# Optimization experiments

Hardware: AMD Instinct MI355X
Metric: run time of the kernel (lower is better)

## Reference

```python
import jax, jax.numpy as jnp
import numpy as np

N, E, IN, HID, H, OUT = 50000, 800000, 128, 64, 4, 128
NEG = 0.2   # LeakyReLU slope in GATv2
EPS = 1e-5  # BatchNorm eps


def _seg_softmax(a, seg, n):
    # numerically stable softmax over edges grouped by destination node
    amax = jax.lax.stop_gradient(jax.ops.segment_max(a, seg, num_segments=n))
    amax = jnp.where(jnp.isfinite(amax), amax, 0.0)
    ex = jnp.exp(a - amax[seg])
    den = jax.ops.segment_sum(ex, seg, num_segments=n)
    return ex / (den[seg] + 1e-16)


def _gatv2(x, src, dst, e_attr, Wl, bl, Wr, br, We, att, bias, heads, c, concat):
    n = x.shape[0]
    xl = (x @ Wl + bl).reshape(n, heads, c)   # source transform (x_j)
    xr = (x @ Wr + br).reshape(n, heads, c)   # target transform (x_i)
    ee = (e_attr @ We).reshape(-1, heads, c)  # edge feature transform
    m = xl[src] + xr[dst] + ee                # [E, H, C]
    m = jnp.where(m > 0, m, NEG * m)          # LeakyReLU
    alpha = _seg_softmax(jnp.einsum('ehc,hc->eh', m, att), dst, n)  # [E, H]
    out = jax.ops.segment_sum(alpha[:, :, None] * xl[src], dst, num_segments=n)
    out = out.reshape(n, heads * c) if concat else out.mean(axis=1)
    return out + bias


def _bn(h, g, b):  # BatchNorm1d, training-mode batch stats (biased var)
    mu = jnp.mean(h, axis=0)
    var = jnp.var(h, axis=0)
    return (h - mu) * jax.lax.rsqrt(var + EPS) * g + b


def _prelu(h, a):
    return jnp.where(h > 0, h, a * h)


def setup_inputs() -> dict:
    key = jax.random.key(0)
    ks = jax.random.split(key, 16)
    def nrm(k, shape, fan):
        return jax.random.normal(k, shape, jnp.float32) / np.float32(np.sqrt(fan))
    x = jax.random.normal(ks[0], (N, IN), jnp.float32)
    edge_index = jax.random.randint(ks[1], (2, E), 0, N, jnp.int32)
    edge_attr = jax.random.uniform(ks[2], (E, 1), dtype=jnp.float32)
    return {
        'x': x, 'edge_index': edge_index, 'edge_attr': edge_attr,
        # layer 1: heads=4, concat=True
        'Wl1': nrm(ks[3], (IN, H * HID), IN), 'bl1': jnp.zeros((H * HID,), jnp.float32),
        'Wr1': nrm(ks[4], (IN, H * HID), IN), 'br1': jnp.zeros((H * HID,), jnp.float32),
        'We1': nrm(ks[5], (1, H * HID), 1),
        'att1': nrm(ks[6], (H, HID), HID),
        'cb1': jnp.zeros((H * HID,), jnp.float32),
        'bng1': jnp.ones((H * HID,), jnp.float32), 'bnb1': jnp.zeros((H * HID,), jnp.float32),
        'pa': jnp.float32(0.25),  # PReLU single parameter (shared by both uses)
        # layer 2: heads=1, concat=False
        'Wl2': nrm(ks[7], (H * HID, OUT), H * HID), 'bl2': jnp.zeros((OUT,), jnp.float32),
        'Wr2': nrm(ks[8], (H * HID, OUT), H * HID), 'br2': jnp.zeros((OUT,), jnp.float32),
        'We2': nrm(ks[9], (1, OUT), 1),
        'att2': nrm(ks[10], (1, OUT), OUT),
        'cb2': jnp.zeros((OUT,), jnp.float32),
        'bng2': jnp.ones((OUT,), jnp.float32), 'bnb2': jnp.zeros((OUT,), jnp.float32),
        'skipW': nrm(ks[11], (IN, OUT), IN), 'skipb': jnp.zeros((OUT,), jnp.float32),
    }


def reference(x, edge_index, edge_attr, Wl1, bl1, Wr1, br1, We1, att1, cb1,
              bng1, bnb1, pa, Wl2, bl2, Wr2, br2, We2, att2, cb2, bng2, bnb2,
              skipW, skipb):
    src, dst = edge_index[0], edge_index[1]
    h = _gatv2(x, src, dst, edge_attr, Wl1, bl1, Wr1, br1, We1, att1, cb1, H, HID, True)
    h = _prelu(_bn(h, bng1, bnb1), pa)  # dropout = identity (eval)
    h = _gatv2(h, src, dst, edge_attr, Wl2, bl2, Wr2, br2, We2, att2, cb2, 1, OUT, False)
    h = _prelu(_bn(h, bng2, bnb2), pa)
    return h + (x @ skipW + skipb)
```

## Files before the change

### kernel.cpp

```cpp
#include <hip/hip_runtime.h>
#include <cstdint>
#include <cstddef>

#define NNODES 50000
#define NEDGES 800000
#define DH1    256
#define DOUT   128

typedef unsigned short u16;
typedef __bf16 bf16x8 __attribute__((ext_vector_type(8)));
typedef float  f32x4  __attribute__((ext_vector_type(4)));

__device__ __forceinline__ float bf2f(unsigned int u) {
  union { unsigned int i; float f; } x; x.i = u << 16; return x.f;
}
__device__ __forceinline__ u16 f2bf(float f) {
  union { float f; unsigned int i; } x; x.f = f;
  unsigned int r = x.i + 0x7fffu + ((x.i >> 16) & 1u);
  return (u16)(r >> 16);
}
__device__ __forceinline__ void dec8(uint4 r, float* o) {
  o[0] = bf2f(r.x & 0xffffu); o[1] = bf2f(r.x >> 16);
  o[2] = bf2f(r.y & 0xffffu); o[3] = bf2f(r.y >> 16);
  o[4] = bf2f(r.z & 0xffffu); o[5] = bf2f(r.z >> 16);
  o[6] = bf2f(r.w & 0xffffu); o[7] = bf2f(r.w >> 16);
}
__device__ __forceinline__ uint4 pack8(const float* v) {
  uint4 p;
  p.x = (unsigned)f2bf(v[0]) | ((unsigned)f2bf(v[1]) << 16);
  p.y = (unsigned)f2bf(v[2]) | ((unsigned)f2bf(v[3]) << 16);
  p.z = (unsigned)f2bf(v[4]) | ((unsigned)f2bf(v[5]) << 16);
  p.w = (unsigned)f2bf(v[6]) | ((unsigned)f2bf(v[7]) << 16);
  return p;
}


__global__ __launch_bounds__(256) void count_k(const int* __restrict__ dst, int* __restrict__ cnt) {
  int e = blockIdx.x * 256 + threadIdx.x;
  if (e < NEDGES) atomicAdd(&cnt[dst[e]], 1);
}

__global__ __launch_bounds__(256) void offsets_k(const int* __restrict__ cnt, int* __restrict__ offs,
                                                 int* __restrict__ cursor, int* __restrict__ total) {
  int i = blockIdx.x * 256 + threadIdx.x;
  int lane = threadIdx.x & 63;
  int c = (i < NNODES) ? cnt[i] : 0;
  int incl = c;
  #pragma unroll
  for (int d = 1; d < 64; d <<= 1) {
    int t = __shfl_up(incl, d, 64);
    if (lane >= d) incl += t;
  }
  int wtotal = __shfl(incl, 63, 64);
  int base = 0;
  if (lane == 63) base = atomicAdd(total, wtotal);
  base = __shfl(base, 63, 64);
  int off = base + incl - c;
  if (i < NNODES) { offs[i] = off; cursor[i] = off; }
}

__global__ __launch_bounds__(256) void scatter_k(const int* __restrict__ src, const int* __restrict__ dst,
                                                 const float* __restrict__ ea, int* __restrict__ cursor,
                                                 int2* __restrict__ epair) {
  int e = blockIdx.x * 256 + threadIdx.x;
  if (e >= NEDGES) return;
  int d = dst[e];
  int p = atomicAdd(&cursor[d], 1);
  int2 v; v.x = src[e]; v.y = __float_as_int(ea[e]);
  epair[p] = v;
}


__global__ __launch_bounds__(256) void cvt_bf_k(const float* __restrict__ in, u16* __restrict__ out, int total) {
  int i = (blockIdx.x * 256 + threadIdx.x) * 4;
  if (i >= total) return;
  float4 v = *reinterpret_cast<const float4*>(in + i);
  uint2 pk;
  pk.x = (unsigned)f2bf(v.x) | ((unsigned)f2bf(v.y) << 16);
  pk.y = (unsigned)f2bf(v.z) | ((unsigned)f2bf(v.w) << 16);
  *reinterpret_cast<uint2*>(out + i) = pk;
}

__global__ __launch_bounds__(256) void prep_all_k(
    const float* __restrict__ Wl1, const float* __restrict__ Wr1,
    const float* __restrict__ bl1, const float* __restrict__ br1,
    const float* __restrict__ Wl2, const float* __restrict__ Wr2,
    const float* __restrict__ bl2, const float* __restrict__ br2,
    const float* __restrict__ skW, const float* __restrict__ skb,
    u16* __restrict__ Wt1, float* __restrict__ bias1,
    u16* __restrict__ Wt2, float* __restrict__ bias2,
    u16* __restrict__ Wts, float* __restrict__ biasS) {
  int idx = blockIdx.x * 256 + threadIdx.x;
  int which = blockIdx.y;
  if (which == 0) {
    if (idx < 512) bias1[idx] = (idx < 256) ? bl1[idx] : br1[idx - 256];
    int n = idx >> 7, k = idx & 127;
    float v = (n < 256) ? Wl1[k * 256 + n] : Wr1[k * 256 + (n - 256)];
    Wt1[idx] = f2bf(v);
  } else if (which == 1) {
    if (idx < 256) bias2[idx] = (idx < 128) ? bl2[idx] : br2[idx - 128];
    int n = idx >> 8, k = idx & 255;
    float v = (n < 128) ? Wl2[k * 128 + n] : Wr2[k * 128 + (n - 128)];
    Wt2[idx] = f2bf(v);
  } else {
    if (idx < 128) biasS[idx] = skb[idx];
    if (idx < 128 * 128) {
      int n = idx >> 7, k = idx & 127;
      Wts[idx] = f2bf(skW[k * 128 + n]);
    }
  }
}


template<int K, int NH, int NTOT, bool OUT_BF16>
__global__ __launch_bounds__(512) void gemm_mfma(
    const u16* __restrict__ A, const u16* __restrict__ Wt, const float* __restrict__ bias,
    void* __restrict__ C0v, void* __restrict__ C1v) {
  constexpr int LDA = K + 8;
  constexpr int LD1 = (NTOT - NH) > 0 ? (NTOT - NH) : 1;
  constexpr int CSTR = OUT_BF16 ? 136 : 132;
  constexpr size_t ABYTES = (size_t)64 * LDA * 2;
  constexpr size_t CBYTES = (size_t)64 * CSTR * (OUT_BF16 ? 2 : 4);
  constexpr size_t SBYTES = ABYTES > CBYTES ? ABYTES : CBYTES;
  __shared__ __align__(16) char smem[SBYTES];
  u16* As = (u16*)smem;
  const int row0 = blockIdx.x * 64;
  const int tid = threadIdx.x;
  #pragma unroll
  for (int it = 0; it < K / 32; ++it) {
    int chunk = it * 512 + tid;
    int row = (chunk * 4) / K;
    int col = (chunk * 4) % K;
    uint2 v; v.x = 0u; v.y = 0u;
    int gr = row0 + row;
    if (gr < NNODES) v = *reinterpret_cast<const uint2*>(A + (size_t)gr * K + col);
    *reinterpret_cast<uint2*>(&As[row * LDA + col]) = v;
  }
  __syncthreads();
  const int w = tid >> 6, lane = tid & 63, q = lane >> 4, l16 = lane & 15;
  const int tc = w * 16 + l16;
  const int ncol = blockIdx.y * 128 + tc;
  f32x4 acc[4];
  #pragma unroll
  for (int rt = 0; rt < 4; ++rt) acc[rt] = (f32x4){0.f, 0.f, 0.f, 0.f};
  const u16* wp = Wt + (size_t)ncol * K + q * 8;
  #pragma unroll
  for (int ks = 0; ks < K / 32; ++ks) {
    bf16x8 b = *reinterpret_cast<const bf16x8*>(wp + ks * 32);
    #pragma unroll
    for (int rt = 0; rt < 4; ++rt) {
      bf16x8 a = *reinterpret_cast<const bf16x8*>(&As[(rt * 16 + l16) * LDA + ks * 32 + q * 8]);
      acc[rt] = __builtin_amdgcn_mfma_f32_16x16x32_bf16(a, b, acc[rt], 0, 0, 0);
    }
  }
  const float bval = bias[ncol];
  __syncthreads();
  if constexpr (OUT_BF16) {
    u16* Cs = (u16*)smem;
    #pragma unroll
    for (int rt = 0; rt < 4; ++rt)
      #pragma unroll
      for (int r = 0; r < 4; ++r)
        Cs[(rt * 16 + q * 4 + r) * CSTR + tc] = f2bf(acc[rt][r] + bval);
  } else {
    float* Cs = (float*)smem;
    #pragma unroll
    for (int rt = 0; rt < 4; ++rt)
      #pragma unroll
      for (int r = 0; r < 4; ++r)
        Cs[(rt * 16 + q * 4 + r) * CSTR + tc] = acc[rt][r] + bval;
  }
  __syncthreads();
  const int cb = blockIdx.y * 128;
  const bool first = (cb < NH);
  const int LD = first ? NH : LD1;
  const int cc = first ? cb : (cb - NH);
  if constexpr (OUT_BF16) {
    u16* Cg = (u16*)(first ? C0v : C1v);
    constexpr int CPR = 16;
    #pragma unroll
    for (int it = 0; it < 64 * CPR / 512; ++it) {
      int ch = it * 512 + tid;
      int row = ch / CPR, co = (ch % CPR) * 8;
      int grow = row0 + row;
      if (grow < NNODES) {
        uint4 v = *reinterpret_cast<const uint4*>(&((u16*)smem)[row * CSTR + co]);
        *reinterpret_cast<uint4*>(Cg + (size_t)grow * LD + cc + co) = v;
      }
    }
  } else {
    float* Cg = (float*)(first ? C0v : C1v);
    constexpr int CPR = 32;
    #pragma unroll
    for (int it = 0; it < 64 * CPR / 512; ++it) {
      int ch = it * 512 + tid;
      int row = ch / CPR, co = (ch % CPR) * 4;
      int grow = row0 + row;
      if (grow < NNODES) {
        float4 v = *reinterpret_cast<const float4*>(&((float*)smem)[row * CSTR + co]);
        *reinterpret_cast<float4*>(Cg + (size_t)grow * LD + cc + co) = v;
      }
    }
  }
}


template<int HEADS, int CHAN>
__global__ __launch_bounds__(256) void gat_edge(
    const int* __restrict__ offs, const int* __restrict__ cnt,
    const int2* __restrict__ epair,
    const u16* __restrict__ xl, const u16* __restrict__ xr,
    const float* __restrict__ att, const float* __restrict__ We,
    const float* __restrict__ cb, u16* __restrict__ hout) {
  constexpr int HC  = HEADS * CHAN;
  constexpr int CPL = HC / 16;
  constexpr int NCH = CPL / 8;
  constexpr int LPH = CHAN / CPL;
  static_assert(NCH * 8 == CPL && LPH * CPL == CHAN, "layout");

  int node = __builtin_amdgcn_readfirstlane((int)(blockIdx.x * 4 + (threadIdx.x >> 6)));
  if (node >= NNODES) return;
  const int lane = threadIdx.x & 63;
  const int g    = lane >> 4;
  const int l16  = lane & 15;
  const int cbase = l16 * CPL;

  float xrv[CPL], attv[CPL], wev[CPL];
  {
    const uint4* xrp = reinterpret_cast<const uint4*>(xr + (size_t)node * HC + cbase);
    #pragma unroll
    for (int c = 0; c < NCH; ++c) dec8(xrp[c], &xrv[c * 8]);
    #pragma unroll
    for (int c = 0; c < CPL / 4; ++c) {
      float4 a = *reinterpret_cast<const float4*>(att + cbase + c * 4);
      float4 w = *reinterpret_cast<const float4*>(We  + cbase + c * 4);
      attv[c*4+0] = a.x; attv[c*4+1] = a.y; attv[c*4+2] = a.z; attv[c*4+3] = a.w;
      wev [c*4+0] = w.x; wev [c*4+1] = w.y; wev [c*4+2] = w.z; wev [c*4+3] = w.w;
    }
  }
  const int off = __builtin_amdgcn_readfirstlane(offs[node]);
  const int deg = __builtin_amdgcn_readfirstlane(cnt[node]);

  float den = 0.f;
  float accv[CPL];
  #pragma unroll
  for (int j = 0; j < CPL; ++j) accv[j] = 0.f;

  if (deg > 0) {
    const int last = deg - 1;
    auto midx = [&](int i) { int j = i * 4 + g; return off + (j < last ? j : last); };
    auto rowp = [&](int s) { return reinterpret_cast<const uint4*>(xl + (size_t)s * HC + cbase); };
    const int niter = (deg + 3) >> 2;
    int2 p_cur = epair[midx(0)];
    int2 p_nxt = epair[midx(1)];
    uint4 r_cur[NCH], r_nxt[NCH];
    { const uint4* rp = rowp(p_cur.x);
      #pragma unroll
      for (int c = 0; c < NCH; ++c) r_cur[c] = rp[c]; }
    for (int i = 0; i < niter; ++i) {
      int2 p_n2 = epair[midx(i + 2)];
      { const uint4* rp = rowp(p_nxt.x);
        #pragma unroll
        for (int c = 0; c < NCH; ++c) r_nxt[c] = rp[c]; }
      float ea = __int_as_float(p_cur.y);
      float xlv[CPL];
      #pragma unroll
      for (int c = 0; c < NCH; ++c) dec8(r_cur[c], &xlv[c * 8]);
      float part = 0.f;
      #pragma unroll
      for (int jj = 0; jj < CPL; ++jj) {
        float m = xlv[jj] + xrv[jj] + ea * wev[jj];
        m = m > 0.f ? m : 0.2f * m;
        part += m * attv[jj];
      }
      #pragma unroll
      for (int d = 1; d < LPH; d <<= 1) part += __shfl_xor(part, d, 64);
      float valid = (i * 4 + g <= last) ? 1.f : 0.f;
      float e = __expf(part) * valid;
      den += e;
      #pragma unroll
      for (int jj = 0; jj < CPL; ++jj) accv[jj] += e * xlv[jj];
      p_cur = p_nxt; p_nxt = p_n2;
      #pragma unroll
      for (int c = 0; c < NCH; ++c) r_cur[c] = r_nxt[c];
    }
  }
  den += __shfl_xor(den, 16, 64);
  den += __shfl_xor(den, 32, 64);
  #pragma unroll
  for (int jj = 0; jj < CPL; ++jj) {
    accv[jj] += __shfl_xor(accv[jj], 16, 64);
    accv[jj] += __shfl_xor(accv[jj], 32, 64);
  }
  if (g == 0) {
    float inv = 1.0f / (den + 1e-16f);
    float ov[CPL];
    #pragma unroll
    for (int c = 0; c < CPL / 4; ++c) {
      float4 cv = *reinterpret_cast<const float4*>(cb + cbase + c * 4);
      ov[c*4+0] = accv[c*4+0] * inv + cv.x;
      ov[c*4+1] = accv[c*4+1] * inv + cv.y;
      ov[c*4+2] = accv[c*4+2] * inv + cv.z;
      ov[c*4+3] = accv[c*4+3] * inv + cv.w;
    }
    uint4* op = reinterpret_cast<uint4*>(hout + (size_t)node * HC + cbase);
    #pragma unroll
    for (int c = 0; c < NCH; ++c) op[c] = pack8(&ov[c * 8]);
  }
}


template<int NC>
__global__ void bn_stats_bf(const u16* __restrict__ h, float* __restrict__ sum, float* __restrict__ sq) {
  int c = threadIdx.x;
  float s = 0.f, q = 0.f;
  for (int r = blockIdx.x; r < NNODES; r += gridDim.x) {
    float v = bf2f(h[(size_t)r * NC + c]);
    s += v; q += v * v;
  }
  atomicAdd(&sum[c], s);
  atomicAdd(&sq[c], q);
}

template<int NC>
__global__ __launch_bounds__(256) void bn_prelu_apply(
    const u16* __restrict__ h, const float* __restrict__ sum, const float* __restrict__ sq,
    const float* __restrict__ g, const float* __restrict__ bb_,
    const float* __restrict__ pap, u16* __restrict__ outp, int total) {
  int i = (blockIdx.x * 256 + threadIdx.x) * 4;
  if (i >= total) return;
  const float invN = 1.0f / (float)NNODES;
  float pa = pap[0];
  int c = i & (NC - 1);
  float4 sm = *reinterpret_cast<const float4*>(sum + c);
  float4 qq = *reinterpret_cast<const float4*>(sq + c);
  float4 gg = *reinterpret_cast<const float4*>(g + c);
  float4 bb = *reinterpret_cast<const float4*>(bb_ + c);
  float mu, var, sc[4], sh[4];
  mu = sm.x * invN; var = qq.x * invN - mu * mu; sc[0] = gg.x * rsqrtf(var + 1e-5f); sh[0] = bb.x - mu * sc[0];
  mu = sm.y * invN; var = qq.y * invN - mu * mu; sc[1] = gg.y * rsqrtf(var + 1e-5f); sh[1] = bb.y - mu * sc[1];
  mu = sm.z * invN; var = qq.z * invN - mu * mu; sc[2] = gg.z * rsqrtf(var + 1e-5f); sh[2] = bb.z - mu * sc[2];
  mu = sm.w * invN; var = qq.w * invN - mu * mu; sc[3] = gg.w * rsqrtf(var + 1e-5f); sh[3] = bb.w - mu * sc[3];
  uint2 raw = *reinterpret_cast<const uint2*>(h + i);
  float v0 = bf2f(raw.x & 0xffffu), v1 = bf2f(raw.x >> 16);
  float v2 = bf2f(raw.y & 0xffffu), v3 = bf2f(raw.y >> 16);
  float o0 = v0 * sc[0] + sh[0]; o0 = o0 > 0.f ? o0 : pa * o0;
  float o1 = v1 * sc[1] + sh[1]; o1 = o1 > 0.f ? o1 : pa * o1;
  float o2 = v2 * sc[2] + sh[2]; o2 = o2 > 0.f ? o2 : pa * o2;
  float o3 = v3 * sc[3] + sh[3]; o3 = o3 > 0.f ? o3 : pa * o3;
  uint2 pk;
  pk.x = (unsigned)f2bf(o0) | ((unsigned)f2bf(o1) << 16);
  pk.y = (unsigned)f2bf(o2) | ((unsigned)f2bf(o3) << 16);
  *reinterpret_cast<uint2*>(outp + i) = pk;
}

__global__ __launch_bounds__(256) void final_out_k(
    const u16* __restrict__ h2, const float* __restrict__ skip,
    const float* __restrict__ sum, const float* __restrict__ sq,
    const float* __restrict__ g, const float* __restrict__ bb_,
    const float* __restrict__ pap, float* __restrict__ outp, int total) {
  int i = (blockIdx.x * 256 + threadIdx.x) * 4;
  if (i >= total) return;
  const float invN = 1.0f / (float)NNODES;
  float pa = pap[0];
  int c = i & 127;
  float4 sm = *reinterpret_cast<const float4*>(sum + c);
  float4 qq = *reinterpret_cast<const float4*>(sq + c);
  float4 gg = *reinterpret_cast<const float4*>(g + c);
  float4 bb = *reinterpret_cast<const float4*>(bb_ + c);
  float mu, var, sc[4], sh[4];
  mu = sm.x * invN; var = qq.x * invN - mu * mu; sc[0] = gg.x * rsqrtf(var + 1e-5f); sh[0] = bb.x - mu * sc[0];
  mu = sm.y * invN; var = qq.y * invN - mu * mu; sc[1] = gg.y * rsqrtf(var + 1e-5f); sh[1] = bb.y - mu * sc[1];
  mu = sm.z * invN; var = qq.z * invN - mu * mu; sc[2] = gg.z * rsqrtf(var + 1e-5f); sh[2] = bb.z - mu * sc[2];
  mu = sm.w * invN; var = qq.w * invN - mu * mu; sc[3] = gg.w * rsqrtf(var + 1e-5f); sh[3] = bb.w - mu * sc[3];
  uint2 raw = *reinterpret_cast<const uint2*>(h2 + i);
  float v0 = bf2f(raw.x & 0xffffu), v1 = bf2f(raw.x >> 16);
  float v2 = bf2f(raw.y & 0xffffu), v3 = bf2f(raw.y >> 16);
  float4 sk = *reinterpret_cast<const float4*>(skip + i);
  float4 o;
  o.x = v0 * sc[0] + sh[0]; o.x = (o.x > 0.f ? o.x : pa * o.x) + sk.x;
  o.y = v1 * sc[1] + sh[1]; o.y = (o.y > 0.f ? o.y : pa * o.y) + sk.y;
  o.z = v2 * sc[2] + sh[2]; o.z = (o.z > 0.f ? o.z : pa * o.z) + sk.z;
  o.w = v3 * sc[3] + sh[3]; o.w = (o.w > 0.f ? o.w : pa * o.w) + sk.w;
  *reinterpret_cast<float4*>(outp + i) = o;
}


extern "C" void kernel_launch(void* const* d_in, const int* in_sizes, int n_in,
                              void* d_out, int out_size, void* d_ws, size_t ws_size,
                              hipStream_t stream) {
  (void)in_sizes; (void)n_in; (void)out_size; (void)ws_size;
  const float* x    = (const float*)d_in[0];
  const int*   ei   = (const int*)d_in[1];
  const float* ea   = (const float*)d_in[2];
  const float* Wl1  = (const float*)d_in[3];
  const float* bl1  = (const float*)d_in[4];
  const float* Wr1  = (const float*)d_in[5];
  const float* br1  = (const float*)d_in[6];
  const float* We1  = (const float*)d_in[7];
  const float* att1 = (const float*)d_in[8];
  const float* cb1  = (const float*)d_in[9];
  const float* bng1 = (const float*)d_in[10];
  const float* bnb1 = (const float*)d_in[11];
  const float* pa   = (const float*)d_in[12];
  const float* Wl2  = (const float*)d_in[13];
  const float* bl2  = (const float*)d_in[14];
  const float* Wr2  = (const float*)d_in[15];
  const float* br2  = (const float*)d_in[16];
  const float* We2  = (const float*)d_in[17];
  const float* att2 = (const float*)d_in[18];
  const float* cb2  = (const float*)d_in[19];
  const float* bng2 = (const float*)d_in[20];
  const float* bnb2 = (const float*)d_in[21];
  const float* skW  = (const float*)d_in[22];
  const float* skb  = (const float*)d_in[23];
  const int* srcp = ei;
  const int* dstp = ei + NEDGES;

  char* base = (char*)d_ws;
  size_t off = 0;
  auto alloc = [&](size_t bytes) -> char* {
    char* p = base + off;
    off = (off + bytes + 255) & ~(size_t)255;
    return p;
  };
  size_t zero_ints = 1 + NNODES + 256 + 256 + 128 + 128;
  char* zbase = alloc(zero_ints * 4);
  int*   totalp = (int*)zbase;
  int*   cnt    = totalp + 1;
  float* bnsum1 = (float*)(cnt + NNODES);
  float* bnsq1  = bnsum1 + 256;
  float* bnsum2 = bnsq1 + 256;
  float* bnsq2  = bnsum2 + 128;

  int*   offs    = (int*)alloc((size_t)NNODES * 4);
  int*   cursor  = (int*)alloc((size_t)NNODES * 4);
  int2*  epair   = (int2*)alloc((size_t)NEDGES * 8);
  const size_t RBYTES = (size_t)NNODES * DH1 * 2;
  char* regionA = alloc(RBYTES);
  char* regionB = alloc(RBYTES);
  char* regionC = alloc(RBYTES);
  u16*   xbf    = (u16*)alloc((size_t)NNODES * 128 * 2);
  u16*   Wt1    = (u16*)alloc(512 * 128 * 2);
  u16*   Wt2    = (u16*)alloc(256 * 256 * 2);
  u16*   Wts    = (u16*)alloc(128 * 128 * 2);
  float* bias1  = (float*)alloc(512 * 4);
  float* bias2  = (float*)alloc(256 * 4);
  float* biasS  = (float*)alloc(128 * 4);

  u16*   xl1     = (u16*)regionA;
  u16*   xr1     = (u16*)regionB;
  u16*   h1      = (u16*)regionC;
  u16*   h1p     = (u16*)regionA;
  u16*   xl2     = (u16*)regionC;
  u16*   xr2     = (u16*)(regionC + (size_t)NNODES * DOUT * 2);
  float* skipbuf = (float*)regionB;
  u16*   h2      = (u16*)regionA;

  hipMemsetAsync(zbase, 0, zero_ints * 4, stream);

  const int EB = (NEDGES + 255) / 256;
  const int NB = (NNODES + 255) / 256;
  count_k<<<EB, 256, 0, stream>>>(dstp, cnt);
  offsets_k<<<NB, 256, 0, stream>>>(cnt, offs, cursor, totalp);
  scatter_k<<<EB, 256, 0, stream>>>(srcp, dstp, ea, cursor, epair);

  cvt_bf_k<<<(NNODES * 128 / 4 + 255) / 256, 256, 0, stream>>>(x, xbf, NNODES * 128);
  prep_all_k<<<dim3(256, 3), 256, 0, stream>>>(Wl1, Wr1, bl1, br1, Wl2, Wr2, bl2, br2,
                                               skW, skb, Wt1, bias1, Wt2, bias2, Wts, biasS);

  const int MB64 = (NNODES + 63) / 64;
  gemm_mfma<128, 256, 512, true><<<dim3(MB64, 4), 512, 0, stream>>>(
      xbf, Wt1, bias1, (void*)xl1, (void*)xr1);
  gat_edge<4, 64><<<(NNODES + 3) / 4, 256, 0, stream>>>(
      offs, cnt, epair, xl1, xr1, att1, We1, cb1, h1);
  bn_stats_bf<256><<<800, 256, 0, stream>>>(h1, bnsum1, bnsq1);
  bn_prelu_apply<256><<<(NNODES * DH1 / 4 + 255) / 256, 256, 0, stream>>>(
      h1, bnsum1, bnsq1, bng1, bnb1, pa, h1p, NNODES * DH1);

  gemm_mfma<256, 128, 256, true><<<dim3(MB64, 2), 512, 0, stream>>>(
      h1p, Wt2, bias2, (void*)xl2, (void*)xr2);
  gemm_mfma<128, 128, 128, false><<<dim3(MB64, 1), 512, 0, stream>>>(
      xbf, Wts, biasS, (void*)skipbuf, (void*)skipbuf);
  gat_edge<1, 128><<<(NNODES + 3) / 4, 256, 0, stream>>>(
      offs, cnt, epair, xl2, xr2, att2, We2, cb2, h2);
  bn_stats_bf<128><<<800, 128, 0, stream>>>(h2, bnsum2, bnsq2);
  final_out_k<<<(NNODES * DOUT / 4 + 255) / 256, 256, 0, stream>>>(
      h2, skipbuf, bnsum2, bnsq2, bng2, bnb2, pa, (float*)d_out, NNODES * DOUT);
}
```

Baseline: 520.4 us.

## Split LeakyReLU attention algebraically, fuse setup kernels and skip GEMM

Measured after the change: 491.9 us. 5.5% less time.

```diff
diff --git a/kernel.cpp b/kernel.cpp
--- a/kernel.cpp
+++ b/kernel.cpp
@@ -35,10 +35,60 @@
 }
 
 
-__global__ __launch_bounds__(256) void count_k(const int* __restrict__ dst, int* __restrict__ cnt) {
-  int e = blockIdx.x * 256 + threadIdx.x;
-  if (e < NEDGES) atomicAdd(&cnt[dst[e]], 1);
-}
+#define CNT_BLKS 3125
+#define CVT_BLKS 6250
+#define W1_BLKS  320
+#define W2_BLKS  256
+
+__global__ __launch_bounds__(256) void setup_k(
+    const int* __restrict__ dst, int* __restrict__ cnt,
+    const float* __restrict__ x, u16* __restrict__ xbf,
+    const float* __restrict__ Wl1, const float* __restrict__ Wr1,
+    const float* __restrict__ bl1, const float* __restrict__ br1,
+    const float* __restrict__ Wl2, const float* __restrict__ Wr2,
+    const float* __restrict__ bl2, const float* __restrict__ br2,
+    const float* __restrict__ skW, const float* __restrict__ skb,
+    const float* __restrict__ att1, const float* __restrict__ We1,
+    const float* __restrict__ att2, const float* __restrict__ We2,
+    u16* __restrict__ Wcat1, float* __restrict__ bias1,
+    u16* __restrict__ Wt2, float* __restrict__ bias2,
+    float* __restrict__ axw) {
+  int b = blockIdx.x, t = threadIdx.x;
+  if (b < CNT_BLKS) {
+    int e = b * 256 + t;
+    if (e < NEDGES) atomicAdd(&cnt[dst[e]], 1);
+  } else if (b < CNT_BLKS + CVT_BLKS) {
+    int i = ((b - CNT_BLKS) * 256 + t) * 4;
+    float4 v = *reinterpret_cast<const float4*>(x + i);
+    uint2 pk;
+    pk.x = (unsigned)f2bf(v.x) | ((unsigned)f2bf(v.y) << 16);
+    pk.y = (unsigned)f2bf(v.z) | ((unsigned)f2bf(v.w) << 16);
+    *reinterpret_cast<uint2*>(xbf + i) = pk;
+  } else if (b < CNT_BLKS + CVT_BLKS + W1_BLKS) {
+    int idx = (b - CNT_BLKS - CVT_BLKS) * 256 + t;
+    if (idx < 640) bias1[idx] = idx < 256 ? bl1[idx] : idx < 512 ? br1[idx - 256] : skb[idx - 512];
+    int n = idx >> 7, k = idx & 127;
+    float v = n < 256 ? Wl1[k * 256 + n] : n < 512 ? Wr1[k * 256 + (n - 256)] : skW[k * 128 + (n - 512)];
+    Wcat1[idx] = f2bf(v);
+  } else if (b < CNT_BLKS + CVT_BLKS + W1_BLKS + W2_BLKS) {
+    int idx = (b - CNT_BLKS - CVT_BLKS - W1_BLKS) * 256 + t;
+    if (idx < 256) bias2[idx] = idx < 128 ? bl2[idx] : br2[idx - 128];
+    int n = idx >> 8, k = idx & 255;
+    float v = n < 128 ? Wl2[k * 128 + n] : Wr2[k * 128 + (n - 128)];
+    Wt2[idx] = f2bf(v);
+  } else {
+    if (t < 4) {
+      float s = 0.f;
+      for (int c = 0; c < 64; ++c) s += att1[t * 64 + c] * We1[t * 64 + c];
+      axw[t] = s;
+    } else if (t == 4) {
+      float s = 0.f;
+      for (int c = 0; c < 128; ++c) s += att2[c] * We2[c];
+      axw[4] = s;
+    }
+  }
+}
+
 
 __global__ __launch_bounds__(256) void offsets_k(const int* __restrict__ cnt, int* __restrict__ offs,
                                                  int* __restrict__ cursor, int* __restrict__ total) {
@@ -71,58 +121,18 @@
 }
 
 
-__global__ __launch_bounds__(256) void cvt_bf_k(const float* __restrict__ in, u16* __restrict__ out, int total) {
-  int i = (blockIdx.x * 256 + threadIdx.x) * 4;
-  if (i >= total) return;
-  float4 v = *reinterpret_cast<const float4*>(in + i);
-  uint2 pk;
-  pk.x = (unsigned)f2bf(v.x) | ((unsigned)f2bf(v.y) << 16);
-  pk.y = (unsigned)f2bf(v.z) | ((unsigned)f2bf(v.w) << 16);
-  *reinterpret_cast<uint2*>(out + i) = pk;
-}
-
-__global__ __launch_bounds__(256) void prep_all_k(
-    const float* __restrict__ Wl1, const float* __restrict__ Wr1,
-    const float* __restrict__ bl1, const float* __restrict__ br1,
-    const float* __restrict__ Wl2, const float* __restrict__ Wr2,
-    const float* __restrict__ bl2, const float* __restrict__ br2,
-    const float* __restrict__ skW, const float* __restrict__ skb,
-    u16* __restrict__ Wt1, float* __restrict__ bias1,
-    u16* __restrict__ Wt2, float* __restrict__ bias2,
-    u16* __restrict__ Wts, float* __restrict__ biasS) {
-  int idx = blockIdx.x * 256 + threadIdx.x;
-  int which = blockIdx.y;
-  if (which == 0) {
-    if (idx < 512) bias1[idx] = (idx < 256) ? bl1[idx] : br1[idx - 256];
-    int n = idx >> 7, k = idx & 127;
-    float v = (n < 256) ? Wl1[k * 256 + n] : Wr1[k * 256 + (n - 256)];
-    Wt1[idx] = f2bf(v);
-  } else if (which == 1) {
-    if (idx < 256) bias2[idx] = (idx < 128) ? bl2[idx] : br2[idx - 128];
-    int n = idx >> 8, k = idx & 255;
-    float v = (n < 128) ? Wl2[k * 128 + n] : Wr2[k * 128 + (n - 128)];
-    Wt2[idx] = f2bf(v);
-  } else {
-    if (idx < 128) biasS[idx] = skb[idx];
-    if (idx < 128 * 128) {
-      int n = idx >> 7, k = idx & 127;
-      Wts[idx] = f2bf(skW[k * 128 + n]);
-    }
-  }
-}
-
-
-template<int K, int NH, int NTOT, bool OUT_BF16>
+template<int K, int B1, int B2, int LDC0, int LDC1, int LDC2, int SPAN, int ATTLEN, bool DO_ATT>
 __global__ __launch_bounds__(512) void gemm_mfma(
     const u16* __restrict__ A, const u16* __restrict__ Wt, const float* __restrict__ bias,
-    void* __restrict__ C0v, void* __restrict__ C1v) {
+    u16* __restrict__ C0, u16* __restrict__ C1, u16* __restrict__ C2,
+    const float* __restrict__ att, float* __restrict__ axl, float* __restrict__ axr) {
   constexpr int LDA = K + 8;
-  constexpr int LD1 = (NTOT - NH) > 0 ? (NTOT - NH) : 1;
-  constexpr int CSTR = OUT_BF16 ? 136 : 132;
+  constexpr int CSTR = 136;
   constexpr size_t ABYTES = (size_t)64 * LDA * 2;
-  constexpr size_t CBYTES = (size_t)64 * CSTR * (OUT_BF16 ? 2 : 4);
+  constexpr size_t CBYTES = (size_t)64 * CSTR * 2;
   constexpr size_t SBYTES = ABYTES > CBYTES ? ABYTES : CBYTES;
   __shared__ __align__(16) char smem[SBYTES];
+  __shared__ float attS[128];
   u16* As = (u16*)smem;
   const int row0 = blockIdx.x * 64;
   const int tid = threadIdx.x;
@@ -139,7 +149,8 @@
   __syncthreads();
   const int w = tid >> 6, lane = tid & 63, q = lane >> 4, l16 = lane & 15;
   const int tc = w * 16 + l16;
-  const int ncol = blockIdx.y * 128 + tc;
+  const int cb = blockIdx.y * 128;
+  const int ncol = cb + tc;
   f32x4 acc[4];
   #pragma unroll
   for (int rt = 0; rt < 4; ++rt) acc[rt] = (f32x4){0.f, 0.f, 0.f, 0.f};
@@ -155,157 +166,152 @@
   }
   const float bval = bias[ncol];
   __syncthreads();
-  if constexpr (OUT_BF16) {
-    u16* Cs = (u16*)smem;
+  u16* Cs = (u16*)smem;
+  #pragma unroll
+  for (int rt = 0; rt < 4; ++rt)
     #pragma unroll
-    for (int rt = 0; rt < 4; ++rt)
-      #pragma unroll
-      for (int r = 0; r < 4; ++r)
-        Cs[(rt * 16 + q * 4 + r) * CSTR + tc] = f2bf(acc[rt][r] + bval);
-  } else {
-    float* Cs = (float*)smem;
+    for (int r = 0; r < 4; ++r)
+      Cs[(rt * 16 + q * 4 + r) * CSTR + tc] = f2bf(acc[rt][r] + bval);
+  __syncthreads();
+  {
+    u16* Cg; int LD, cc;
+    if (cb < B1)      { Cg = C0; LD = LDC0; cc = cb; }
+    else if (cb < B2) { Cg = C1; LD = LDC1; cc = cb - B1; }
+    else              { Cg = C2; LD = LDC2; cc = cb - B2; }
     #pragma unroll
-    for (int rt = 0; rt < 4; ++rt)
-      #pragma unroll
-      for (int r = 0; r < 4; ++r)
-        Cs[(rt * 16 + q * 4 + r) * CSTR + tc] = acc[rt][r] + bval;
-  }
-  __syncthreads();
-  const int cb = blockIdx.y * 128;
-  const bool first = (cb < NH);
-  const int LD = first ? NH : LD1;
-  const int cc = first ? cb : (cb - NH);
-  if constexpr (OUT_BF16) {
-    u16* Cg = (u16*)(first ? C0v : C1v);
-    constexpr int CPR = 16;
-    #pragma unroll
-    for (int it = 0; it < 64 * CPR / 512; ++it) {
+    for (int it = 0; it < 2; ++it) {
       int ch = it * 512 + tid;
-      int row = ch / CPR, co = (ch % CPR) * 8;
+      int row = ch / 16, co = (ch % 16) * 8;
       int grow = row0 + row;
       if (grow < NNODES) {
-        uint4 v = *reinterpret_cast<const uint4*>(&((u16*)smem)[row * CSTR + co]);
+        uint4 v = *reinterpret_cast<const uint4*>(&Cs[row * CSTR + co]);
         *reinterpret_cast<uint4*>(Cg + (size_t)grow * LD + cc + co) = v;
       }
     }
-  } else {
-    float* Cg = (float*)(first ? C0v : C1v);
-    constexpr int CPR = 32;
-    #pragma unroll
-    for (int it = 0; it < 64 * CPR / 512; ++it) {
-      int ch = it * 512 + tid;
-      int row = ch / CPR, co = (ch % CPR) * 4;
-      int grow = row0 + row;
-      if (grow < NNODES) {
-        float4 v = *reinterpret_cast<const float4*>(&((float*)smem)[row * CSTR + co]);
-        *reinterpret_cast<float4*>(Cg + (size_t)grow * LD + cc + co) = v;
+  }
+  if constexpr (DO_ATT) {
+    if (cb < B2) {
+      if (tid < 128) attS[tid] = att[(cb + tid) % ATTLEN];
+      __syncthreads();
+      constexpr int TPR = 128 / SPAN;
+      constexpr int HEADS = B1 / SPAN;
+      if (tid < 64 * TPR) {
+        int row = tid / TPR, hb = tid % TPR;
+        const u16* cr = Cs + row * CSTR + hb * SPAN;
+        float s = 0.f;
+        for (int c = 0; c < SPAN; ++c) s += bf2f(cr[c]) * attS[hb * SPAN + c];
+        int grow = row0 + row;
+        if (grow < NNODES) {
+          int cbl = cb < B1 ? cb : cb - B1;
+          int lh = cbl / SPAN + hb;
+          float* dstp = (cb < B1) ? axl : axr;
+          dstp[grow * HEADS + lh] = s;
+        }
       }
     }
   }
 }
 
 
-template<int HEADS, int CHAN>
+template<int HEADS, int CHAN, int EPW>
 __global__ __launch_bounds__(256) void gat_edge(
     const int* __restrict__ offs, const int* __restrict__ cnt,
     const int2* __restrict__ epair,
     const u16* __restrict__ xl, const u16* __restrict__ xr,
     const float* __restrict__ att, const float* __restrict__ We,
-    const float* __restrict__ cb, u16* __restrict__ hout) {
+    const float* __restrict__ cb,
+    const float* __restrict__ axl, const float* __restrict__ axr,
+    const float* __restrict__ aWep, u16* __restrict__ hout) {
   constexpr int HC  = HEADS * CHAN;
-  constexpr int CPL = HC / 16;
-  constexpr int NCH = CPL / 8;
+  constexpr int GSZ = 64 / EPW;
+  constexpr int CPL = HC / GSZ;
   constexpr int LPH = CHAN / CPL;
-  static_assert(NCH * 8 == CPL && LPH * CPL == CHAN, "layout");
+  static_assert(CPL == 8, "layout");
 
   int node = __builtin_amdgcn_readfirstlane((int)(blockIdx.x * 4 + (threadIdx.x >> 6)));
   if (node >= NNODES) return;
   const int lane = threadIdx.x & 63;
-  const int g    = lane >> 4;
-  const int l16  = lane & 15;
-  const int cbase = l16 * CPL;
-
-  float xrv[CPL], attv[CPL], wev[CPL];
+  const int g    = lane / GSZ;
+  const int lgs  = lane & (GSZ - 1);
+  const int h    = lgs / LPH;
+  const int cbase = lgs * CPL;
+
+  float xrv[8], attv[8], wev[8];
   {
-    const uint4* xrp = reinterpret_cast<const uint4*>(xr + (size_t)node * HC + cbase);
-    #pragma unroll
-    for (int c = 0; c < NCH; ++c) dec8(xrp[c], &xrv[c * 8]);
-    #pragma unroll
-    for (int c = 0; c < CPL / 4; ++c) {
-      float4 a = *reinterpret_cast<const float4*>(att + cbase + c * 4);
-      float4 w = *reinterpret_cast<const float4*>(We  + cbase + c * 4);
-      attv[c*4+0] = a.x; attv[c*4+1] = a.y; attv[c*4+2] = a.z; attv[c*4+3] = a.w;
-      wev [c*4+0] = w.x; wev [c*4+1] = w.y; wev [c*4+2] = w.z; wev [c*4+3] = w.w;
-    }
-  }
+    uint4 xrr = *reinterpret_cast<const uint4*>(xr + (size_t)node * HC + cbase);
+    dec8(xrr, xrv);
+    float4 a0 = *reinterpret_cast<const float4*>(att + cbase);
+    float4 a1 = *reinterpret_cast<const float4*>(att + cbase + 4);
+    float4 w0 = *reinterpret_cast<const float4*>(We + cbase);
+    float4 w1 = *reinterpret_cast<const float4*>(We + cbase + 4);
+    attv[0]=a0.x; attv[1]=a0.y; attv[2]=a0.z; attv[3]=a0.w;
+    attv[4]=a1.x; attv[5]=a1.y; attv[6]=a1.z; attv[7]=a1.w;
+    wev[0]=w0.x; wev[1]=w0.y; wev[2]=w0.z; wev[3]=w0.w;
+    wev[4]=w1.x; wev[5]=w1.y; wev[6]=w1.z; wev[7]=w1.w;
+  }
+  const float aWe = aWep[h];
+  const float axr_n = axr[node * HEADS + h];
   const int off = __builtin_amdgcn_readfirstlane(offs[node]);
   const int deg = __builtin_amdgcn_readfirstlane(cnt[node]);
 
   float den = 0.f;
-  float accv[CPL];
-  #pragma unroll
-  for (int j = 0; j < CPL; ++j) accv[j] = 0.f;
+  float accv[8];
+  #pragma unroll
+  for (int c = 0; c < 8; ++c) accv[c] = 0.f;
 
   if (deg > 0) {
     const int last = deg - 1;
-    auto midx = [&](int i) { int j = i * 4 + g; return off + (j < last ? j : last); };
-    auto rowp = [&](int s) { return reinterpret_cast<const uint4*>(xl + (size_t)s * HC + cbase); };
-    const int niter = (deg + 3) >> 2;
+    auto midx = [&](int i) { int j = i * EPW + g; return off + (j < last ? j : last); };
     int2 p_cur = epair[midx(0)];
     int2 p_nxt = epair[midx(1)];
-    uint4 r_cur[NCH], r_nxt[NCH];
-    { const uint4* rp = rowp(p_cur.x);
-      #pragma unroll
-      for (int c = 0; c < NCH; ++c) r_cur[c] = rp[c]; }
+    uint4 r_cur; float ax_cur;
+    { int s = p_cur.x;
+      r_cur = *reinterpret_cast<const uint4*>(xl + (size_t)s * HC + cbase);
+      ax_cur = axl[s * HEADS + h]; }
+    const int niter = (deg + EPW - 1) / EPW;
     for (int i = 0; i < niter; ++i) {
       int2 p_n2 = epair[midx(i + 2)];
-      { const uint4* rp = rowp(p_nxt.x);
-        #pragma unroll
-        for (int c = 0; c < NCH; ++c) r_nxt[c] = rp[c]; }
+      uint4 r_n; float ax_n;
+      { int s = p_nxt.x;
+        r_n = *reinterpret_cast<const uint4*>(xl + (size_t)s * HC + cbase);
+        ax_n = axl[s * HEADS + h]; }
       float ea = __int_as_float(p_cur.y);
-      float xlv[CPL];
+      float xlv[8];
+      dec8(r_cur, xlv);
+      float part2 = 0.f;
       #pragma unroll
-      for (int c = 0; c < NCH; ++c) dec8(r_cur[c], &xlv[c * 8]);
-      float part = 0.f;
-      #pragma unroll
-      for (int jj = 0; jj < CPL; ++jj) {
-        float m = xlv[jj] + xrv[jj] + ea * wev[jj];
-        m = m > 0.f ? m : 0.2f * m;
-        part += m * attv[jj];
+      for (int c = 0; c < 8; ++c) {
+        float m = xlv[c] + fmaf(ea, wev[c], xrv[c]);
+        part2 = fmaf(fabsf(m), attv[c], part2);
       }
       #pragma unroll
-      for (int d = 1; d < LPH; d <<= 1) part += __shfl_xor(part, d, 64);
-      float valid = (i * 4 + g <= last) ? 1.f : 0.f;
-      float e = __expf(part) * valid;
+      for (int d = 1; d < LPH; d <<= 1) part2 += __shfl_xor(part2, d, 64);
+      float ssum = ax_cur + fmaf(ea, aWe, axr_n);
+      float sc = fmaf(0.4f, part2, 0.6f * ssum);
+      float e = __expf(sc);
+      e = (i * EPW + g <= last) ? e : 0.f;
       den += e;
       #pragma unroll
-      for (int jj = 0; jj < CPL; ++jj) accv[jj] += e * xlv[jj];
-      p_cur = p_nxt; p_nxt = p_n2;
-      #pragma unroll
-      for (int c = 0; c < NCH; ++c) r_cur[c] = r_nxt[c];
+      for (int c = 0; c < 8; ++c) accv[c] = fmaf(e, xlv[c], accv[c]);
+      p_cur = p_nxt; p_nxt = p_n2; r_cur = r_n; ax_cur = ax_n;
     }
   }
-  den += __shfl_xor(den, 16, 64);
-  den += __shfl_xor(den, 32, 64);
-  #pragma unroll
-  for (int jj = 0; jj < CPL; ++jj) {
-    accv[jj] += __shfl_xor(accv[jj], 16, 64);
-    accv[jj] += __shfl_xor(accv[jj], 32, 64);
+  #pragma unroll
+  for (int d = GSZ; d < 64; d <<= 1) {
+    den += __shfl_xor(den, d, 64);
+    #pragma unroll
+    for (int c = 0; c < 8; ++c) accv[c] += __shfl_xor(accv[c], d, 64);
   }
   if (g == 0) {
     float inv = 1.0f / (den + 1e-16f);
-    float ov[CPL];
-    #pragma unroll
-    for (int c = 0; c < CPL / 4; ++c) {
-      float4 cv = *reinterpret_cast<const float4*>(cb + cbase + c * 4);
-      ov[c*4+0] = accv[c*4+0] * inv + cv.x;
-      ov[c*4+1] = accv[c*4+1] * inv + cv.y;
-      ov[c*4+2] = accv[c*4+2] * inv + cv.z;
-      ov[c*4+3] = accv[c*4+3] * inv + cv.w;
-    }
-    uint4* op = reinterpret_cast<uint4*>(hout + (size_t)node * HC + cbase);
-    #pragma unroll
-    for (int c = 0; c < NCH; ++c) op[c] = pack8(&ov[c * 8]);
+    float4 c0 = *reinterpret_cast<const float4*>(cb + cbase);
+    float4 c1 = *reinterpret_cast<const float4*>(cb + cbase + 4);
+    float ov[8];
+    ov[0] = accv[0] * inv + c0.x; ov[1] = accv[1] * inv + c0.y;
+    ov[2] = accv[2] * inv + c0.z; ov[3] = accv[3] * inv + c0.w;
+    ov[4] = accv[4] * inv + c1.x; ov[5] = accv[5] * inv + c1.y;
+    ov[6] = accv[6] * inv + c1.z; ov[7] = accv[7] * inv + c1.w;
+    *reinterpret_cast<uint4*>(hout + (size_t)node * HC + cbase) = pack8(ov);
   }
 }
 
@@ -355,7 +361,7 @@
 }
 
 __global__ __launch_bounds__(256) void final_out_k(
-    const u16* __restrict__ h2, const float* __restrict__ skip,
+    const u16* __restrict__ h2, const u16* __restrict__ skip,
     const float* __restrict__ sum, const float* __restrict__ sq,
     const float* __restrict__ g, const float* __restrict__ bb_,
     const float* __restrict__ pap, float* __restrict__ outp, int total) {
@@ -376,12 +382,14 @@
   uint2 raw = *reinterpret_cast<const uint2*>(h2 + i);
   float v0 = bf2f(raw.x & 0xffffu), v1 = bf2f(raw.x >> 16);
   float v2 = bf2f(raw.y & 0xffffu), v3 = bf2f(raw.y >> 16);
-  float4 sk = *reinterpret_cast<const float4*>(skip + i);
+  uint2 skr = *reinterpret_cast<const uint2*>(skip + i);
+  float s0 = bf2f(skr.x & 0xffffu), s1 = bf2f(skr.x >> 16);
+  float s2 = bf2f(skr.y & 0xffffu), s3 = bf2f(skr.y >> 16);
   float4 o;
-  o.x = v0 * sc[0] + sh[0]; o.x = (o.x > 0.f ? o.x : pa * o.x) + sk.x;
-  o.y = v1 * sc[1] + sh[1]; o.y = (o.y > 0.f ? o.y : pa * o.y) + sk.y;
-  o.z = v2 * sc[2] + sh[2]; o.z = (o.z > 0.f ? o.z : pa * o.z) + sk.z;
-  o.w = v3 * sc[3] + sh[3]; o.w = (o.w > 0.f ? o.w : pa * o.w) + sk.w;
+  o.x = v0 * sc[0] + sh[0]; o.x = (o.x > 0.f ? o.x : pa * o.x) + s0;
+  o.y = v1 * sc[1] + sh[1]; o.y = (o.y > 0.f ? o.y : pa * o.y) + s1;
+  o.z = v2 * sc[2] + sh[2]; o.z = (o.z > 0.f ? o.z : pa * o.z) + s2;
+  o.w = v3 * sc[3] + sh[3]; o.w = (o.w > 0.f ? o.w : pa * o.w) + s3;
   *reinterpret_cast<float4*>(outp + i) = o;
 }
 
@@ -441,12 +449,16 @@
   char* regionB = alloc(RBYTES);
   char* regionC = alloc(RBYTES);
   u16*   xbf    = (u16*)alloc((size_t)NNODES * 128 * 2);
-  u16*   Wt1    = (u16*)alloc(512 * 128 * 2);
+  u16*   skipbf = (u16*)alloc((size_t)NNODES * 128 * 2);
+  u16*   Wcat1  = (u16*)alloc(640 * 128 * 2);
   u16*   Wt2    = (u16*)alloc(256 * 256 * 2);
-  u16*   Wts    = (u16*)alloc(128 * 128 * 2);
-  float* bias1  = (float*)alloc(512 * 4);
+  float* bias1  = (float*)alloc(640 * 4);
   float* bias2  = (float*)alloc(256 * 4);
-  float* biasS  = (float*)alloc(128 * 4);
+  float* axw    = (float*)alloc(8 * 4);
+  float* axl1   = (float*)alloc((size_t)NNODES * 4 * 4);
+  float* axr1   = (float*)alloc((size_t)NNODES * 4 * 4);
+  float* axl2   = (float*)alloc((size_t)NNODES * 4);
+  float* axr2   = (float*)alloc((size_t)NNODES * 4);
 
   u16*   xl1     = (u16*)regionA;
   u16*   xr1     = (u16*)regionB;
@@ -454,37 +466,32 @@
   u16*   h1p     = (u16*)regionA;
   u16*   xl2     = (u16*)regionC;
   u16*   xr2     = (u16*)(regionC + (size_t)NNODES * DOUT * 2);
-  float* skipbuf = (float*)regionB;
   u16*   h2      = (u16*)regionA;
 
   hipMemsetAsync(zbase, 0, zero_ints * 4, stream);
 
   const int EB = (NEDGES + 255) / 256;
   const int NB = (NNODES + 255) / 256;
-  count_k<<<EB, 256, 0, stream>>>(dstp, cnt);
+  setup_k<<<CNT_BLKS + CVT_BLKS + W1_BLKS + W2_BLKS + 1, 256, 0, stream>>>(
+      dstp, cnt, x, xbf, Wl1, Wr1, bl1, br1, Wl2, Wr2, bl2, br2, skW, skb,
+      att1, We1, att2, We2, Wcat1, bias1, Wt2, bias2, axw);
   offsets_k<<<NB, 256, 0, stream>>>(cnt, offs, cursor, totalp);
   scatter_k<<<EB, 256, 0, stream>>>(srcp, dstp, ea, cursor, epair);
 
-  cvt_bf_k<<<(NNODES * 128 / 4 + 255) / 256, 256, 0, stream>>>(x, xbf, NNODES * 128);
-  prep_all_k<<<dim3(256, 3), 256, 0, stream>>>(Wl1, Wr1, bl1, br1, Wl2, Wr2, bl2, br2,
-                                               skW, skb, Wt1, bias1, Wt2, bias2, Wts, biasS);
-
   const int MB64 = (NNODES + 63) / 64;
-  gemm_mfma<128, 256, 512, true><<<dim3(MB64, 4), 512, 0, stream>>>(
-      xbf, Wt1, bias1, (void*)xl1, (void*)xr1);
-  gat_edge<4, 64><<<(NNODES + 3) / 4, 256, 0, stream>>>(
-      offs, cnt, epair, xl1, xr1, att1, We1, cb1, h1);
+  gemm_mfma<128, 256, 512, 256, 256, 128, 64, 256, true><<<dim3(MB64, 5), 512, 0, stream>>>(
+      xbf, Wcat1, bias1, xl1, xr1, skipbf, att1, axl1, axr1);
+  gat_edge<4, 64, 2><<<(NNODES + 3) / 4, 256, 0, stream>>>(
+      offs, cnt, epair, xl1, xr1, att1, We1, cb1, axl1, axr1, axw, h1);
   bn_stats_bf<256><<<800, 256, 0, stream>>>(h1, bnsum1, bnsq1);
   bn_prelu_apply<256><<<(NNODES * DH1 / 4 + 255) / 256, 256, 0, stream>>>(
       h1, bnsum1, bnsq1, bng1, bnb1, pa, h1p, NNODES * DH1);
 
-  gemm_mfma<256, 128, 256, true><<<dim3(MB64, 2), 512, 0, stream>>>(
-      h1p, Wt2, bias2, (void*)xl2, (void*)xr2);
-  gemm_mfma<128, 128, 128, false><<<dim3(MB64, 1), 512, 0, stream>>>(
-      xbf, Wts, biasS, (void*)skipbuf, (void*)skipbuf);
-  gat_edge<1, 128><<<(NNODES + 3) / 4, 256, 0, stream>>>(
-      offs, cnt, epair, xl2, xr2, att2, We2, cb2, h2);
+  gemm_mfma<256, 128, 256, 128, 128, 1, 128, 128, true><<<dim3(MB64, 2), 512, 0, stream>>>(
+      h1p, Wt2, bias2, xl2, xr2, (u16*)0, att2, axl2, axr2);
+  gat_edge<1, 128, 4><<<(NNODES + 3) / 4, 256, 0, stream>>>(
+      offs, cnt, epair, xl2, xr2, att2, We2, cb2, axl2, axr2, axw + 4, h2);
   bn_stats_bf<128><<<800, 128, 0, stream>>>(h2, bnsum2, bnsq2);
   final_out_k<<<(NNODES * DOUT / 4 + 255) / 256, 256, 0, stream>>>(
-      h2, skipbuf, bnsum2, bnsq2, bng2, bnb2, pa, (float*)d_out, NNODES * DOUT);
-}
+      h2, skipbf, bnsum2, bnsq2, bng2, bnb2, pa, (float*)d_out, NNODES * DOUT);
+}
```
